# Performance work log

Hardware: AMD Instinct MI355X
Metric: run time of the kernel (lower is better)

The kernel has to match this reference:

```python
import jax, jax.numpy as jnp
import numpy as np

NUM_HEADS = 4
SCALE = 0.17677669529663687  # head_dim(32) ** -0.5


def setup_inputs() -> dict:
    key = jax.random.key(0)
    k1, k2 = jax.random.split(key)
    qkv = jax.random.normal(k1, (1024, 144, 384), dtype=jnp.float32)
    mask = jax.random.normal(k2, (1, 4, 144, 144), dtype=jnp.float32)
    return {"qkv": qkv, "mask": mask}


def reference(qkv, mask):
    B, N, C = qkv.shape
    hd = C // NUM_HEADS // 3  # head_dim = 32
    # [B,N,3,H,hd] -> [3,B,H,N,hd]
    qkv = qkv.reshape(B, N, 3, NUM_HEADS, hd).transpose(2, 0, 3, 1, 4)
    q, k, v = qkv[0] * SCALE, qkv[1], qkv[2]
    attn = jnp.einsum("bhqd,bhkd->bhqk", q, k) + mask  # mask broadcasts over B
    attn = jax.nn.softmax(attn, axis=-1)
    out = jnp.einsum("bhqk,bhkd->bhqd", attn, v)  # [B,H,N,hd]
    return out.transpose(0, 2, 1, 3).reshape(B, N, C // 3)
```

## Files before the change

### kernel.cpp

```cpp
#include <hip/hip_runtime.h>
#include <hip/hip_bf16.h>
#include <stdint.h>

#define NB 1024
#define NN 144
#define NH 4
#define HDIM 32
#define CC 384
#define SCALE_F 0.17677669529663687f

#define KSTR 40
#define VSTR 168
#define PSTR 168

typedef __attribute__((ext_vector_type(8))) short short8;
typedef __attribute__((ext_vector_type(4))) float float4v;

__device__ __forceinline__ uint16_t f2b(float f) {
    __hip_bfloat16 h = __float2bfloat16(f);
    return *reinterpret_cast<uint16_t*>(&h);
}

__global__ __launch_bounds__(192, 3) void attn_kernel(
    const float* __restrict__ qkv,
    const float* __restrict__ mask,
    float* __restrict__ out)
{
    __shared__ __align__(16) uint16_t Kl[NN * KSTR];
    __shared__ __align__(16) uint16_t Vt[HDIM * VSTR];
    __shared__ __align__(16) uint16_t Pb[3 * 16 * PSTR];

    const int bid  = blockIdx.x;
    const int b    = ((bid >> 5) << 3) | (bid & 7);
    const int h    = (bid >> 3) & 3;
    const int tid  = threadIdx.x;
    const int wave = tid >> 6;
    const int lane = tid & 63;
    const int col  = lane & 15;
    const int quad = lane >> 4;

    const float* qkv_b = qkv + (size_t)b * (NN * CC);

    for (int idx = tid; idx < NN * 8; idx += 192) {
        const int ki = idx >> 3;
        const int g  = idx & 7;
        float4 kv = *(const float4*)(qkv_b + ki * CC + 128 + h * HDIM + g * 4);
        ushort4 kp;
        kp.x = f2b(kv.x); kp.y = f2b(kv.y); kp.z = f2b(kv.z); kp.w = f2b(kv.w);
        *(ushort4*)&Kl[ki * KSTR + g * 4] = kp;

        float4 vv = *(const float4*)(qkv_b + ki * CC + 256 + h * HDIM + g * 4);
        const int d0 = g * 4;
        Vt[(d0 + 0) * VSTR + ki] = f2b(vv.x);
        Vt[(d0 + 1) * VSTR + ki] = f2b(vv.y);
        Vt[(d0 + 2) * VSTR + ki] = f2b(vv.z);
        Vt[(d0 + 3) * VSTR + ki] = f2b(vv.w);
    }
    for (int i = tid; i < HDIM * 16; i += 192)
        Vt[(i >> 4) * VSTR + NN + (i & 15)] = 0;
    uint16_t* Pw = &Pb[wave * 16 * PSTR];
    for (int i = lane; i < 16 * 16; i += 64)
        Pw[(i >> 4) * PSTR + NN + (i & 15)] = 0;

    __syncthreads();

    const float* mbase = mask + h * (NN * NN);
    const float4v zf = {0.f, 0.f, 0.f, 0.f};

    short8 ones;
    #pragma unroll
    for (int j = 0; j < 8; j++) ones[j] = (short)0x3F80;

    for (int s = wave; s < 9; s += 3) {
        const int qi0 = s * 16;

        float mreg[9][4];
        #pragma unroll
        for (int t = 0; t < 9; t++) {
            #pragma unroll
            for (int r = 0; r < 4; r++)
                mreg[t][r] = mbase[(qi0 + quad * 4 + r) * NN + t * 16 + col];
        }

        const float* qp = qkv_b + (size_t)(qi0 + col) * CC + h * HDIM + quad * 8;
        float4 q0 = ((const float4*)qp)[0];
        float4 q1 = ((const float4*)qp)[1];
        short8 qfrag;
        qfrag[0] = (short)f2b(q0.x); qfrag[1] = (short)f2b(q0.y);
        qfrag[2] = (short)f2b(q0.z); qfrag[3] = (short)f2b(q0.w);
        qfrag[4] = (short)f2b(q1.x); qfrag[5] = (short)f2b(q1.y);
        qfrag[6] = (short)f2b(q1.z); qfrag[7] = (short)f2b(q1.w);

        float4v S[9];
        #pragma unroll
        for (int t = 0; t < 9; t++) {
            short8 kfrag = *(const short8*)&Kl[(t * 16 + col) * KSTR + quad * 8];
            S[t] = __builtin_amdgcn_mfma_f32_16x16x32_bf16(qfrag, kfrag, zf, 0, 0, 0);
        }

        #pragma unroll
        for (int t = 0; t < 9; t++) {
            #pragma unroll
            for (int r = 0; r < 4; r++) {
                float p = __expf(fmaf(S[t][r], SCALE_F, mreg[t][r]));
                Pw[(quad * 4 + r) * PSTR + t * 16 + col] = f2b(p);
            }
        }

        float4v O0 = zf, O1 = zf, L = zf;
        #pragma unroll
        for (int kt = 0; kt < 5; kt++) {
            short8 pfrag = *(const short8*)&Pw[col * PSTR + kt * 32 + quad * 8];
            short8 vf0   = *(const short8*)&Vt[col * VSTR + kt * 32 + quad * 8];
            short8 vf1   = *(const short8*)&Vt[(16 + col) * VSTR + kt * 32 + quad * 8];
            O0 = __builtin_amdgcn_mfma_f32_16x16x32_bf16(pfrag, vf0, O0, 0, 0, 0);
            O1 = __builtin_amdgcn_mfma_f32_16x16x32_bf16(pfrag, vf1, O1, 0, 0, 0);
            L  = __builtin_amdgcn_mfma_f32_16x16x32_bf16(pfrag, ones, L, 0, 0, 0);
        }

        float* ob = out + ((size_t)b * NN + qi0) * 128 + h * HDIM;
        #pragma unroll
        for (int r = 0; r < 4; r++) {
            float inv = 1.0f / L[r];
            int orow = (quad * 4 + r) * 128;
            ob[orow + col]      = O0[r] * inv;
            ob[orow + 16 + col] = O1[r] * inv;
        }
    }
}

extern "C" void kernel_launch(void* const* d_in, const int* in_sizes, int n_in,
                              void* d_out, int out_size, void* d_ws, size_t ws_size,
                              hipStream_t stream) {
    const float* qkv  = (const float*)d_in[0];
    const float* mask = (const float*)d_in[1];
    float* out        = (float*)d_out;
    attn_kernel<<<dim3(NB * NH), dim3(192), 0, stream>>>(qkv, mask, out);
}
```

Before: 343.0 us.

## Batch K/V/Q global loads up front and prefetch next mask tile

Issues all K/V loads into registers before converting them and writing shared memory, and preloads the Q fragments for all three strips, so global load latency overlaps instead of being serialized per loop iteration. The mask tile for the next strip is loaded right after the current softmax consumes mreg, overlapping with the PV MFMA stage. This raises register pressure (kbuf, vbuf, qbuf held live), which could reduce occupancy under launch_bounds(192,3) or cause spills.

```diff
diff --git a/kernel.cpp b/kernel.cpp
--- a/kernel.cpp
+++ b/kernel.cpp
@@ -40,21 +40,53 @@
     const int quad = lane >> 4;
 
     const float* qkv_b = qkv + (size_t)b * (NN * CC);
+    const float* mbase = mask + h * (NN * NN);
 
-    for (int idx = tid; idx < NN * 8; idx += 192) {
+    float4 kbuf[6], vbuf[6];
+    #pragma unroll
+    for (int i = 0; i < 6; i++) {
+        const int idx = tid + i * 192;
         const int ki = idx >> 3;
         const int g  = idx & 7;
-        float4 kv = *(const float4*)(qkv_b + ki * CC + 128 + h * HDIM + g * 4);
+        kbuf[i] = *(const float4*)(qkv_b + ki * CC + 128 + h * HDIM + g * 4);
+        vbuf[i] = *(const float4*)(qkv_b + ki * CC + 256 + h * HDIM + g * 4);
+    }
+
+    float4 qbuf[3][2];
+    #pragma unroll
+    for (int s3 = 0; s3 < 3; s3++) {
+        const int qi0 = (wave + s3 * 3) * 16;
+        const float* qp = qkv_b + (size_t)(qi0 + col) * CC + h * HDIM + quad * 8;
+        qbuf[s3][0] = ((const float4*)qp)[0];
+        qbuf[s3][1] = ((const float4*)qp)[1];
+    }
+
+    float mreg[9][4];
+    {
+        const int qi0 = wave * 16;
+        #pragma unroll
+        for (int t = 0; t < 9; t++) {
+            #pragma unroll
+            for (int r = 0; r < 4; r++)
+                mreg[t][r] = mbase[(qi0 + quad * 4 + r) * NN + t * 16 + col];
+        }
+    }
+
+    #pragma unroll
+    for (int i = 0; i < 6; i++) {
+        const int idx = tid + i * 192;
+        const int ki = idx >> 3;
+        const int g  = idx & 7;
         ushort4 kp;
-        kp.x = f2b(kv.x); kp.y = f2b(kv.y); kp.z = f2b(kv.z); kp.w = f2b(kv.w);
+        kp.x = f2b(kbuf[i].x); kp.y = f2b(kbuf[i].y);
+        kp.z = f2b(kbuf[i].z); kp.w = f2b(kbuf[i].w);
         *(ushort4*)&Kl[ki * KSTR + g * 4] = kp;
 
-        float4 vv = *(const float4*)(qkv_b + ki * CC + 256 + h * HDIM + g * 4);
         const int d0 = g * 4;
-        Vt[(d0 + 0) * VSTR + ki] = f2b(vv.x);
-        Vt[(d0 + 1) * VSTR + ki] = f2b(vv.y);
-        Vt[(d0 + 2) * VSTR + ki] = f2b(vv.z);
-        Vt[(d0 + 3) * VSTR + ki] = f2b(vv.w);
+        Vt[(d0 + 0) * VSTR + ki] = f2b(vbuf[i].x);
+        Vt[(d0 + 1) * VSTR + ki] = f2b(vbuf[i].y);
+        Vt[(d0 + 2) * VSTR + ki] = f2b(vbuf[i].z);
+        Vt[(d0 + 3) * VSTR + ki] = f2b(vbuf[i].w);
     }
     for (int i = tid; i < HDIM * 16; i += 192)
         Vt[(i >> 4) * VSTR + NN + (i & 15)] = 0;
@@ -64,32 +96,21 @@
 
     __syncthreads();
 
-    const float* mbase = mask + h * (NN * NN);
     const float4v zf = {0.f, 0.f, 0.f, 0.f};
 
     short8 ones;
     #pragma unroll
     for (int j = 0; j < 8; j++) ones[j] = (short)0x3F80;
 
-    for (int s = wave; s < 9; s += 3) {
-        const int qi0 = s * 16;
+    #pragma unroll
+    for (int s3 = 0; s3 < 3; s3++) {
+        const int qi0 = (wave + s3 * 3) * 16;
 
-        float mreg[9][4];
-        #pragma unroll
-        for (int t = 0; t < 9; t++) {
-            #pragma unroll
-            for (int r = 0; r < 4; r++)
-                mreg[t][r] = mbase[(qi0 + quad * 4 + r) * NN + t * 16 + col];
-        }
-
-        const float* qp = qkv_b + (size_t)(qi0 + col) * CC + h * HDIM + quad * 8;
-        float4 q0 = ((const float4*)qp)[0];
-        float4 q1 = ((const float4*)qp)[1];
         short8 qfrag;
-        qfrag[0] = (short)f2b(q0.x); qfrag[1] = (short)f2b(q0.y);
-        qfrag[2] = (short)f2b(q0.z); qfrag[3] = (short)f2b(q0.w);
-        qfrag[4] = (short)f2b(q1.x); qfrag[5] = (short)f2b(q1.y);
-        qfrag[6] = (short)f2b(q1.z); qfrag[7] = (short)f2b(q1.w);
+        qfrag[0] = (short)f2b(qbuf[s3][0].x); qfrag[1] = (short)f2b(qbuf[s3][0].y);
+        qfrag[2] = (short)f2b(qbuf[s3][0].z); qfrag[3] = (short)f2b(qbuf[s3][0].w);
+        qfrag[4] = (short)f2b(qbuf[s3][1].x); qfrag[5] = (short)f2b(qbuf[s3][1].y);
+        qfrag[6] = (short)f2b(qbuf[s3][1].z); qfrag[7] = (short)f2b(qbuf[s3][1].w);
 
         float4v S[9];
         #pragma unroll
@@ -104,6 +125,16 @@
             for (int r = 0; r < 4; r++) {
                 float p = __expf(fmaf(S[t][r], SCALE_F, mreg[t][r]));
                 Pw[(quad * 4 + r) * PSTR + t * 16 + col] = f2b(p);
+            }
+        }
+
+        if (s3 < 2) {
+            const int qn = (wave + (s3 + 1) * 3) * 16;
+            #pragma unroll
+            for (int t = 0; t < 9; t++) {
+                #pragma unroll
+                for (int r = 0; r < 4; r++)
+                    mreg[t][r] = mbase[(qn + quad * 4 + r) * NN + t * 16 + col];
             }
         }
 
```

Result: no change. 337.5 us (-1.6%).
